# Kernel tuning notes

Measured on AMD Instinct MI355X. Metric: run time of the kernel, lower is better.

## Reference

```python
import jax, jax.numpy as jnp
import numpy as np
from jax import lax

# VGG16 conv configuration: (in_ch, out_ch) for 13 3x3 convs, blocks [2,2,3,3,3]
CONV_CFG = [(3,64),(64,64),(64,128),(128,128),(128,256),(256,256),(256,256),(256,512),(512,512),(512,512),(512,512),(512,512),(512,512)]
FC_CFG = [(512*7*7,4096),(4096,4096),(4096,1000)]
BLOCKS = [2,2,3,3,3]

def setup_inputs() -> dict:
    key = jax.random.key(0)
    ks = jax.random.split(key, 40)
    d = {"x": jax.random.normal(ks[0], (16,3,224,224), jnp.float32)}
    for i, (cin, cout) in enumerate(CONV_CFG):
        std = (2.0 / (cin * 9)) ** 0.5  # He init keeps 13-deep ReLU chain stable
        d[f"w{i+1}"] = jax.random.normal(ks[1+i], (cout, cin, 3, 3), jnp.float32) * std
        d[f"b{i+1}"] = jnp.zeros((cout,), jnp.float32)
    for j, (fin, fout) in enumerate(FC_CFG):
        std = (2.0 / fin) ** 0.5
        d[f"fw{j+1}"] = jax.random.normal(ks[20+j], (fin, fout), jnp.float32) * std
        d[f"fb{j+1}"] = jnp.zeros((fout,), jnp.float32)
    d["patch_location_tensor"] = jax.random.randint(ks[30], (16, 2), 0, 200)
    d["p_height"] = 16
    d["p_width"] = 16
    return d

def _conv_relu(x, w, b):
    # 3x3 conv, stride 1, SAME padding (pad=1), NCHW, followed by ReLU
    y = lax.conv_general_dilated(x, w, (1, 1), 'SAME', dimension_numbers=('NCHW', 'OIHW', 'NCHW'))
    return jax.nn.relu(y + b[None, :, None, None])

def _maxpool2(x):
    return lax.reduce_window(x, -jnp.inf, lax.max, (1, 1, 2, 2), (1, 1, 2, 2), 'VALID')

def reference(x, w1, b1, w2, b2, w3, b3, w4, b4, w5, b5, w6, b6, w7, b7, w8, b8, w9, b9, w10, b10, w11, b11, w12, b12, w13, b13, fw1, fb1, fw2, fb2, fw3, fb3, patch_location_tensor, p_height, p_width):
    # The incremental modules patch-update cached full-model activations; the net
    # result equals a dense VGG16 forward on x. patch_location_tensor / p_height /
    # p_width only control which region is recomputed, not the output values.
    ws = [w1, w2, w3, w4, w5, w6, w7, w8, w9, w10, w11, w12, w13]
    bs = [b1, b2, b3, b4, b5, b6, b7, b8, b9, b10, b11, b12, b13]
    h = x
    k = 0
    for n in BLOCKS:
        for _ in range(n):
            h = _conv_relu(h, ws[k], bs[k])
            k += 1
        h = _maxpool2(h)
    h = h.reshape(h.shape[0], -1)  # [B, 25088]
    h = jax.nn.relu(h @ fw1 + fb1)
    h = jax.nn.relu(h @ fw2 + fb2)
    return h @ fw3 + fb3  # [B, 1000]
```

## Files before the change

kernel.cpp:

```cpp
#include <hip/hip_runtime.h>
#include <hip/hip_bf16.h>

typedef __hip_bfloat16 bf16;
typedef __attribute__((ext_vector_type(4))) short s16x4;
typedef __attribute__((ext_vector_type(8))) short short8;
typedef __attribute__((ext_vector_type(8))) __bf16 bf16x8;
typedef __attribute__((ext_vector_type(4))) float f32x4;

__device__ __forceinline__ float s2f(short s) {
  return __builtin_bit_cast(float, (unsigned)((unsigned short)s) << 16);
}
__device__ __forceinline__ short f2s(float f) {
  return __builtin_bit_cast(short, __float2bfloat16(f));
}

__device__ __forceinline__ void gl16(const bf16* g, bf16* l) {
  __builtin_amdgcn_global_load_lds(
      (const __attribute__((address_space(1))) void*)g,
      (__attribute__((address_space(3))) void*)l, 16, 0, 0);
}

__global__ void zerofill(float* p, int n) {
  int i = blockIdx.x * 256 + threadIdx.x;
  if (i < n) p[i] = 0.f;
}

__global__ __launch_bounds__(256) void conv1_first(
    const float* __restrict__ x, const float* __restrict__ w,
    const float* __restrict__ b, bf16* __restrict__ out) {
  __shared__ float it[3][18][18];
  __shared__ float wl2[27 * 64];
  __shared__ float bl[64];
  const int tid = threadIdx.x;
  const int n = blockIdx.z;
  const int h0 = blockIdx.y * 16, w0 = blockIdx.x * 16;
  for (int i = tid; i < 1728; i += 256) {
    int jj = i >> 6, co = i & 63;
    wl2[i] = w[co * 27 + jj];
  }
  if (tid < 64) bl[tid] = b[tid];
  for (int i = tid; i < 972; i += 256) {
    int ci = i / 324; int r = i - ci * 324; int ty = r / 18, tx = r - ty * 18;
    int hh = h0 - 1 + ty, ww = w0 - 1 + tx;
    float v = 0.f;
    if (hh >= 0 && hh < 224 && ww >= 0 && ww < 224)
      v = x[((long)n * 3 + ci) * 50176 + hh * 224 + ww];
    it[ci][ty][tx] = v;
  }
  __syncthreads();
  const int ty = tid >> 4, tx = tid & 15;
  long ob = (((long)n * 224 + h0 + ty) * 224 + (w0 + tx)) * 64;
  for (int cog = 0; cog < 4; ++cog) {
    f32x4 a4[4];
    #pragma unroll
    for (int q = 0; q < 4; ++q) a4[q] = *(const f32x4*)&bl[cog * 16 + q * 4];
    #pragma unroll
    for (int jj = 0; jj < 27; ++jj) {
      const int ci = jj / 9, r = jj - ci * 9, kh = r / 3, kw = r - kh * 3;
      float v = it[ci][ty + kh][tx + kw];
      const f32x4* wp4 = (const f32x4*)&wl2[jj * 64 + cog * 16];
      #pragma unroll
      for (int q = 0; q < 4; ++q) a4[q] += v * wp4[q];
    }
    short8 s0, s1;
    #pragma unroll
    for (int u = 0; u < 4; ++u) {
      s0[u] = f2s(fmaxf(a4[0][u], 0.f));
      s0[4 + u] = f2s(fmaxf(a4[1][u], 0.f));
      s1[u] = f2s(fmaxf(a4[2][u], 0.f));
      s1[4 + u] = f2s(fmaxf(a4[3][u], 0.f));
    }
    *(short8*)(out + ob + cog * 16) = s0;
    *(short8*)(out + ob + cog * 16 + 8) = s1;
  }
}

struct RepackMeta {
  const float* src[12];
  long dstOff[12];
  int cinM1[12];
  int cshift[12];
  int cout[12];
};

__global__ __launch_bounds__(256) void repack_all(RepackMeta m, bf16* __restrict__ blob) {
  const int li = blockIdx.y;
  const int co = blockIdx.x;
  if (co >= m.cout[li]) return;
  const int cs = m.cshift[li];
  const int cinM1 = m.cinM1[li];
  const int K = 9 << cs;
  const float* src = m.src[li] + (long)co * (cinM1 + 1) * 9;
  bf16* dst = blob + m.dstOff[li] + (long)co * K;
  for (int k = threadIdx.x; k < K; k += 256) {
    int pos = k >> cs;
    int ci = k & cinM1;
    dst[k] = __float2bfloat16(src[ci * 9 + pos]);
  }
}

__global__ __launch_bounds__(256) void conv_halo64(
    const bf16* __restrict__ in, const bf16* __restrict__ wp,
    const float* __restrict__ bias, bf16* __restrict__ out,
    const bf16* __restrict__ zp) {
  __shared__ bf16 tA[10 * 34 * 64];
  __shared__ bf16 tB[9 * 64 * 64];
  const int tid = threadIdx.x;
  const int lane = tid & 63, wv = tid >> 6;
  const int n = blockIdx.z;
  const int h0 = blockIdx.y * 8, w0 = blockIdx.x * 32;

  #pragma unroll
  for (int i = 0; i < 11; ++i) {
    int cid = i * 256 + tid;
    if (cid < 2720) {
      int row = cid / 272;
      int rem = cid - row * 272;
      int w = rem >> 3, j = rem & 7;
      int hg = h0 - 1 + row, wg = w0 - 1 + w;
      bool ok = (hg >= 0) & (hg < 224) & (wg >= 0) & (wg < 224);
      const bf16* src = ok ? (in + (((long)n * 224 + hg) * 224 + wg) * 64 + ((j ^ (w & 7)) << 3))
                           : zp;
      gl16(src, tA + (long)cid * 8);
    }
  }
  {
    const int colB = tid >> 3;
    const int colx = ((tid & 7) ^ (colB & 7)) * 8;
    const bf16* s0 = wp + (long)colB * 576 + colx;
    const bf16* s1 = wp + (long)(colB + 32) * 576 + colx;
    #pragma unroll
    for (int p = 0; p < 9; ++p) {
      gl16(s0 + p * 64, tB + p * 4096 + tid * 8);
      gl16(s1 + p * 64, tB + p * 4096 + 2048 + tid * 8);
    }
  }
  __syncthreads();

  f32x4 acc[4][4];
  #pragma unroll
  for (int m = 0; m < 4; ++m)
    #pragma unroll
    for (int n2 = 0; n2 < 4; ++n2) acc[m][n2] = (f32x4){0.f, 0.f, 0.f, 0.f};

  for (int pos = 0; pos < 9; ++pos) {
    const int dh = pos / 3, dw = pos - (pos / 3) * 3;
    #pragma unroll
    for (int ks = 0; ks < 2; ++ks) {
      const int kb = ks * 64 + (lane >> 4) * 16;
      bf16x8 af[4], bfv[4];
      #pragma unroll
      for (int m = 0; m < 4; ++m) {
        int p = wv * 64 + m * 16 + (lane & 15);
        int hl = (p >> 5) + dh, wl = (p & 31) + dw;
        af[m] = *(const bf16x8*)((const char*)tA + hl * 4352 + wl * 128 + (kb ^ ((wl & 7) << 4)));
      }
      #pragma unroll
      for (int n2 = 0; n2 < 4; ++n2) {
        int c = n2 * 16 + (lane & 15);
        bfv[n2] = *(const bf16x8*)((const char*)tB + pos * 8192 + c * 128 + (kb ^ ((c & 7) << 4)));
      }
      #pragma unroll
      for (int m = 0; m < 4; ++m)
        #pragma unroll
        for (int n2 = 0; n2 < 4; ++n2)
          acc[m][n2] = __builtin_amdgcn_mfma_f32_16x16x32_bf16(af[m], bfv[n2], acc[m][n2], 0, 0, 0);
    }
  }

  const int ho = blockIdx.y * 4 + wv;
  #pragma unroll
  for (int m = 0; m < 2; ++m) {
    #pragma unroll
    for (int n2 = 0; n2 < 4; ++n2) {
      int co = n2 * 16 + (lane & 15);
      float bb = bias[co];
      #pragma unroll
      for (int qh = 0; qh < 2; ++qh) {
        int qq = 2 * qh;
        float v0 = fmaxf(acc[m][n2][qq] + bb, 0.f);
        float v1 = fmaxf(acc[m][n2][qq + 1] + bb, 0.f);
        float v2 = fmaxf(acc[m + 2][n2][qq] + bb, 0.f);
        float v3 = fmaxf(acc[m + 2][n2][qq + 1] + bb, 0.f);
        float mx = fmaxf(fmaxf(v0, v1), fmaxf(v2, v3));
        int wl = (m * 16 + ((lane >> 4) << 2) + qq) & 31;
        int wo = (w0 >> 1) + (wl >> 1);
        out[(((long)n * 112 + ho) * 112 + wo) * 64 + co] = __float2bfloat16(mx);
      }
    }
  }
}

__global__ __launch_bounds__(512) void conv_halo128p(
    const bf16* __restrict__ in, const bf16* __restrict__ wp,
    const float* __restrict__ bias, bf16* __restrict__ out,
    const bf16* __restrict__ zp) {
  __shared__ bf16 tA[18 * 18 * 128];
  __shared__ bf16 tB[2][128 * 128];
  const int tid = threadIdx.x;
  const int lane = tid & 63, wv = tid >> 6;
  const int wr = wv >> 1, wc = wv & 1;
  const int n = blockIdx.z;
  const int h0 = blockIdx.y * 16, w0 = blockIdx.x * 16;

  #pragma unroll
  for (int i = 0; i < 11; ++i) {
    int cid = i * 512 + tid;
    if (cid < 5184) {
      int row = cid / 288;
      int rem = cid - row * 288;
      int w = rem >> 4, j = rem & 15;
      int hg = h0 - 1 + row, wg = w0 - 1 + w;
      bool ok = (hg >= 0) & (hg < 112) & (wg >= 0) & (wg < 112);
      const bf16* src = ok ? (in + (((long)n * 112 + hg) * 112 + wg) * 128 + ((j ^ (w & 7)) << 3))
                           : zp;
      gl16(src, tA + (long)cid * 8);
    }
  }
  #pragma unroll
  for (int i = 0; i < 4; ++i) {
    int cid = i * 512 + tid;
    int co = cid >> 4, j = cid & 15;
    const bf16* src = wp + (long)co * 1152 + ((j ^ (co & 7)) << 3);
    gl16(src, tB[0] + (long)cid * 8);
  }
  __syncthreads();

  f32x4 acc[4][4];
  #pragma unroll
  for (int m = 0; m < 4; ++m)
    #pragma unroll
    for (int n2 = 0; n2 < 4; ++n2) acc[m][n2] = (f32x4){0.f, 0.f, 0.f, 0.f};

  for (int pos = 0; pos < 9; ++pos) {
    if (pos < 8) {
      bf16* dst = tB[(pos + 1) & 1];
      #pragma unroll
      for (int i = 0; i < 4; ++i) {
        int cid = i * 512 + tid;
        int co = cid >> 4, j = cid & 15;
        const bf16* src = wp + (long)co * 1152 + (pos + 1) * 128 + ((j ^ (co & 7)) << 3);
        gl16(src, dst + (long)cid * 8);
      }
    }
    const bf16* bB = tB[pos & 1];
    const int dh = pos / 3, dw = pos - (pos / 3) * 3;
    #pragma unroll
    for (int kq = 0; kq < 4; ++kq) {
      const int kb = kq * 64 + (lane >> 4) * 16;
      bf16x8 af[4], bfv[4];
      #pragma unroll
      for (int m = 0; m < 4; ++m) {
        int hl = wr * 4 + m + dh;
        int wl = (lane & 15) + dw;
        af[m] = *(const bf16x8*)((const char*)tA + hl * 4608 + wl * 256 + (kb ^ ((wl & 7) << 4)));
      }
      #pragma unroll
      for (int n2 = 0; n2 < 4; ++n2) {
        int c = wc * 64 + n2 * 16 + (lane & 15);
        bfv[n2] = *(const bf16x8*)((const char*)bB + c * 256 + (kb ^ ((c & 7) << 4)));
      }
      #pragma unroll
      for (int m = 0; m < 4; ++m)
        #pragma unroll
        for (int n2 = 0; n2 < 4; ++n2)
          acc[m][n2] = __builtin_amdgcn_mfma_f32_16x16x32_bf16(af[m], bfv[n2], acc[m][n2], 0, 0, 0);
    }
    __syncthreads();
  }

  const int hoB = blockIdx.y * 8, woB = blockIdx.x * 8;
  #pragma unroll
  for (int mh = 0; mh < 2; ++mh) {
    const int m = 2 * mh;
    const int ho = hoB + wr * 2 + mh;
    #pragma unroll
    for (int n2 = 0; n2 < 4; ++n2) {
      int co = wc * 64 + n2 * 16 + (lane & 15);
      float bb = bias[co];
      #pragma unroll
      for (int qh = 0; qh < 2; ++qh) {
        int qq = 2 * qh;
        float v0 = fmaxf(acc[m][n2][qq] + bb, 0.f);
        float v1 = fmaxf(acc[m][n2][qq + 1] + bb, 0.f);
        float v2 = fmaxf(acc[m + 1][n2][qq] + bb, 0.f);
        float v3 = fmaxf(acc[m + 1][n2][qq + 1] + bb, 0.f);
        float mx = fmaxf(fmaxf(v0, v1), fmaxf(v2, v3));
        int wo = woB + (lane >> 4) * 2 + qh;
        out[(((long)n * 56 + ho) * 56 + wo) * 128 + co] = __float2bfloat16(mx);
      }
    }
  }
}

template <int BM, int BN, int WM, int WN, int SPLITK>
__global__ __launch_bounds__(WM* WN * 64) void conv_gemm(
    const bf16* __restrict__ in, const bf16* __restrict__ wp,
    const float* __restrict__ bias, bf16* __restrict__ out,
    float* __restrict__ pout, const bf16* __restrict__ zp,
    int Cin, int cshift, int Cout, int H, int W, int NHW) {
  constexpr int NT = WM * WN * 64;
  constexpr int IA = BM * 8 / NT;
  constexpr int IB = BN * 8 / NT;
  __shared__ bf16 lA[BM * 64];
  __shared__ bf16 lB[BN * 64];
  const int tid = threadIdx.x;
  const int lane = tid & 63, wv = tid >> 6;
  const int wr = wv / WN, wc = wv % WN;

  const int gx = gridDim.x;
  const int nwg = gx * gridDim.y;
  const int fid = blockIdx.y * gx + blockIdx.x;
  const int q = nwg >> 3, r = nwg & 7;
  const int xcd = fid & 7, idx = fid >> 3;
  const int swz = (xcd < r ? xcd * (q + 1) : r * (q + 1) + (xcd - r) * q) + idx;
  const int p0 = (swz % gx) * BM;
  const int co0 = (swz / gx) * BN;

  const int K = 9 << cshift;
  const int HW = H * W;
  const int colx = ((tid & 7) ^ ((tid >> 3) & 7)) * 8;

  int baseA[IA]; short hA[IA], wA[IA];
  #pragma unroll
  for (int i = 0; i < IA; ++i) {
    int rr = i * (NT / 8) + (tid >> 3);
    int p = p0 + rr;
    if (p < NHW) {
      int n = p / HW; int rem = p - n * HW; int h = rem / W; int w_ = rem - h * W;
      hA[i] = (short)h; wA[i] = (short)w_;
      baseA[i] = ((n * H + h) * W + w_) * Cin;
    } else { hA[i] = -9999; wA[i] = -9999; baseA[i] = 0; }
  }

  f32x4 acc[4][4];
  #pragma unroll
  for (int m = 0; m < 4; ++m)
    #pragma unroll
    for (int n2 = 0; n2 < 4; ++n2) acc[m][n2] = (f32x4){0.f, 0.f, 0.f, 0.f};

  const int Kper = K / SPLITK;
  const int kBeg = (SPLITK > 1) ? (int)blockIdx.z * Kper : 0;
  const int kEnd = kBeg + Kper;

  const bf16* srcB[IB];
  #pragma unroll
  for (int i = 0; i < IB; ++i) {
    int col = i * (NT / 8) + (tid >> 3);
    srcB[i] = wp + (long)(co0 + col) * K + kBeg + colx;
  }

  int kk = kBeg;
  while (kk < kEnd) {
    const int pos = kk >> cshift;
    const int dh = pos / 3 - 1, dw = pos - (pos / 3) * 3 - 1;
    int posEnd = (pos + 1) << cshift;
    if (posEnd > kEnd) posEnd = kEnd;
    const bf16* srcA[IA];
    {
      const int doff = (dh * W + dw) * Cin + (kk & (Cin - 1)) + colx;
      #pragma unroll
      for (int i = 0; i < IA; ++i) {
        int hh = hA[i] + dh, ww = wA[i] + dw;
        bool ok = (hh >= 0) & (hh < H) & (ww >= 0) & (ww < W);
        srcA[i] = ok ? (in + baseA[i] + doff) : (zp + colx);
      }
    }
    for (; kk < posEnd; kk += 64) {
      __syncthreads();
      #pragma unroll
      for (int i = 0; i < IA; ++i) {
        gl16(srcA[i], lA + i * (NT * 8) + wv * 512);
        srcA[i] += 64;
      }
      #pragma unroll
      for (int i = 0; i < IB; ++i) {
        gl16(srcB[i], lB + i * (NT * 8) + wv * 512);
        srcB[i] += 64;
      }
      __syncthreads();
      #pragma unroll
      for (int ks = 0; ks < 2; ++ks) {
        const int kb = ks * 64 + (lane >> 4) * 16;
        bf16x8 af[4], bfv[4];
        #pragma unroll
        for (int m = 0; m < 4; ++m) {
          int rr = wr * 64 + m * 16 + (lane & 15);
          af[m] = *(const bf16x8*)((const char*)lA + rr * 128 + (kb ^ ((rr & 7) << 4)));
        }
        #pragma unroll
        for (int n2 = 0; n2 < 4; ++n2) {
          int c = wc * 64 + n2 * 16 + (lane & 15);
          bfv[n2] = *(const bf16x8*)((const char*)lB + c * 128 + (kb ^ ((c & 7) << 4)));
        }
        #pragma unroll
        for (int m = 0; m < 4; ++m)
          #pragma unroll
          for (int n2 = 0; n2 < 4; ++n2)
            acc[m][n2] = __builtin_amdgcn_mfma_f32_16x16x32_bf16(af[m], bfv[n2], acc[m][n2], 0, 0, 0);
      }
    }
  }

  if constexpr (SPLITK == 1) {
    #pragma unroll
    for (int m = 0; m < 4; ++m) {
      int pb = p0 + wr * 64 + m * 16 + (lane >> 4) * 4;
      #pragma unroll
      for (int n2 = 0; n2 < 4; ++n2) {
        int co = co0 + wc * 64 + n2 * 16 + (lane & 15);
        float bb = bias[co];
        #pragma unroll
        for (int qq = 0; qq < 4; ++qq) {
          int pp = pb + qq;
          if (pp < NHW)
            out[(long)pp * Cout + co] = __float2bfloat16(fmaxf(acc[m][n2][qq] + bb, 0.f));
        }
      }
    }
  } else {
    float* pb_ = pout + (long)blockIdx.z * NHW * Cout;
    #pragma unroll
    for (int m = 0; m < 4; ++m) {
      int pb = p0 + wr * 64 + m * 16 + (lane >> 4) * 4;
      #pragma unroll
      for (int n2 = 0; n2 < 4; ++n2) {
        int co = co0 + wc * 64 + n2 * 16 + (lane & 15);
        #pragma unroll
        for (int qq = 0; qq < 4; ++qq) {
          int pp = pb + qq;
          if (pp < NHW) pb_[(long)pp * Cout + co] = acc[m][n2][qq];
        }
      }
    }
  }
}

template <int NPARTS, bool POOL>
__global__ __launch_bounds__(256) void reduce_split(
    const float* __restrict__ part, const float* __restrict__ bias,
    bf16* __restrict__ out, int NHW, int H, int W, int C) {
  const long total = (long)NHW * C;
  if constexpr (!POOL) {
    long e4 = ((long)blockIdx.x * 256 + threadIdx.x) * 4;
    if (e4 >= total) return;
    f32x4 s = *(const f32x4*)(part + e4);
    #pragma unroll
    for (int p2 = 1; p2 < NPARTS; ++p2) {
      f32x4 b = *(const f32x4*)(part + (long)p2 * total + e4);
      s += b;
    }
    f32x4 bv = *(const f32x4*)(bias + (int)(e4 & (C - 1)));
    s16x4 r;
    #pragma unroll
    for (int u = 0; u < 4; ++u) r[u] = f2s(fmaxf(s[u] + bv[u], 0.f));
    *(s16x4*)(out + e4) = r;
  } else {
    const int H2 = H >> 1, W2 = W >> 1;
    long id4 = ((long)blockIdx.x * 256 + threadIdx.x) * 4;
    long ptotal = ((long)NHW / 4) * C;
    if (id4 >= ptotal) return;
    int c4 = (int)(id4 & (C - 1));
    long rest = id4 / C;
    int wo = (int)(rest % W2);
    long t2 = rest / W2;
    int ho = (int)(t2 % H2);
    int n = (int)(t2 / H2);
    f32x4 bv = *(const f32x4*)(bias + c4);
    f32x4 mx;
    #pragma unroll
    for (int dy = 0; dy < 2; ++dy)
      #pragma unroll
      for (int dx = 0; dx < 2; ++dx) {
        long p = ((long)n * H + 2 * ho + dy) * W + 2 * wo + dx;
        long e = p * C + c4;
        f32x4 s = *(const f32x4*)(part + e);
        #pragma unroll
        for (int p2 = 1; p2 < NPARTS; ++p2) {
          f32x4 b = *(const f32x4*)(part + (long)p2 * total + e);
          s += b;
        }
        s += bv;
        if (dy == 0 && dx == 0) mx = s;
        else {
          #pragma unroll
          for (int u = 0; u < 4; ++u) mx[u] = fmaxf(mx[u], s[u]);
        }
      }
    s16x4 r;
    #pragma unroll
    for (int u = 0; u < 4; ++u) r[u] = f2s(fmaxf(mx[u], 0.f));
    *(s16x4*)(out + ((long)(n * H2 + ho) * W2 + wo) * C + c4) = r;
  }
}

__global__ void maxpool_nhwc(const bf16* __restrict__ in, bf16* __restrict__ out,
                             int H, int W, int C, int cshift3, int WC8) {
  const int id = blockIdx.x * 256 + threadIdx.x;
  if (id >= WC8) return;
  const int H2 = H >> 1, W2 = W >> 1;
  const int ho = blockIdx.y, n = blockIdx.z;
  const int wo = id >> cshift3, c8 = id & ((1 << cshift3) - 1);
  const bf16* p = in + (((long)(n * H + 2 * ho) * W) + 2 * wo) * C + c8 * 8;
  short8 a = *(const short8*)p;
  short8 bq = *(const short8*)(p + C);
  short8 c = *(const short8*)(p + (long)W * C);
  short8 d = *(const short8*)(p + (long)W * C + C);
  short8 r;
  #pragma unroll
  for (int u = 0; u < 8; ++u) {
    float m = fmaxf(fmaxf(s2f(a[u]), s2f(bq[u])), fmaxf(s2f(c[u]), s2f(d[u])));
    r[u] = f2s(m);
  }
  *(short8*)(out + ((long)(n * H2 + ho) * W2 + wo) * C + c8 * 8) = r;
}

__global__ __launch_bounds__(256) void fc1_partial(
    const bf16* __restrict__ in, const float* __restrict__ w,
    float* __restrict__ part) {
  const int j0 = blockIdx.x * 1024 + threadIdx.x * 4;
  const int k0 = blockIdx.y * 128;
  __shared__ float ilds[128][16];
  #pragma unroll
  for (int i = 0; i < 8; ++i) {
    int e = i * 256 + threadIdx.x;
    int kk = e >> 4, n = e & 15;
    int k = k0 + kk;
    int cch = k / 49, s = k - cch * 49;
    ilds[kk][n] = s2f(__builtin_bit_cast(short, in[((long)n * 49 + s) * 512 + cch]));
  }
  __syncthreads();
  f32x4 acc[16];
  #pragma unroll
  for (int n = 0; n < 16; ++n) acc[n] = (f32x4){0.f, 0.f, 0.f, 0.f};
  #pragma unroll 4
  for (int kk = 0; kk < 128; ++kk) {
    f32x4 w4 = *(const f32x4*)(w + (long)(k0 + kk) * 4096 + j0);
    #pragma unroll
    for (int n = 0; n < 16; ++n) {
      float v = ilds[kk][n];
      acc[n] += v * w4;
    }
  }
  float* pp = part + (long)blockIdx.y * 16 * 4096;
  #pragma unroll
  for (int n = 0; n < 16; ++n) *(f32x4*)(pp + n * 4096 + j0) = acc[n];
}

template <int KPER>
__global__ __launch_bounds__(256) void fc23_partial(
    const float* __restrict__ in, const float* __restrict__ w,
    float* __restrict__ part, int fin, int fout) {
  const int j0 = blockIdx.x * 1024 + threadIdx.x * 4;
  const int k0 = blockIdx.y * KPER;
  __shared__ float ilds[KPER][16];
  #pragma unroll
  for (int i = 0; i < KPER / 16; ++i) {
    int e = i * 256 + threadIdx.x;
    int kk = e >> 4, n = e & 15;
    ilds[kk][n] = fmaxf(in[(long)n * fin + k0 + kk], 0.f);
  }
  __syncthreads();
  if (j0 >= fout) return;
  f32x4 acc[16];
  #pragma unroll
  for (int n = 0; n < 16; ++n) acc[n] = (f32x4){0.f, 0.f, 0.f, 0.f};
  #pragma unroll 4
  for (int kk = 0; kk < KPER; ++kk) {
    f32x4 w4 = *(const f32x4*)(w + (long)(k0 + kk) * fout + j0);
    #pragma unroll
    for (int n = 0; n < 16; ++n) {
      float v = ilds[kk][n];
      acc[n] += v * w4;
    }
  }
  float* pp = part + (long)blockIdx.y * 16 * fout;
  #pragma unroll
  for (int n = 0; n < 16; ++n) *(f32x4*)(pp + n * fout + j0) = acc[n];
}

__global__ void reduce_fc(const float* __restrict__ part, const float* __restrict__ bias,
                          float* __restrict__ out, int nparts, int fout, int total) {
  int i = blockIdx.x * 256 + threadIdx.x;
  if (i >= total) return;
  int n = i / fout, j = i - n * fout;
  float s = bias[j];
  for (int p = 0; p < nparts; ++p) s += part[((long)p * 16 + n) * fout + j];
  out[i] = s;
}

extern "C" void kernel_launch(void* const* d_in, const int* in_sizes, int n_in,
                              void* d_out, int out_size, void* d_ws, size_t ws_size,
                              hipStream_t stream) {
  const float* x = (const float*)d_in[0];
  const float* cw[13]; const float* cb[13];
  for (int i = 0; i < 13; ++i) { cw[i] = (const float*)d_in[1 + 2 * i]; cb[i] = (const float*)d_in[2 + 2 * i]; }
  const float* fw1 = (const float*)d_in[27]; const float* fb1 = (const float*)d_in[28];
  const float* fw2 = (const float*)d_in[29]; const float* fb2 = (const float*)d_in[30];
  const float* fw3 = (const float*)d_in[31]; const float* fb3 = (const float*)d_in[32];
  float* outp = (float*)d_out;

  const size_t REGION = 102760448;
  char* wsb = (char*)d_ws;
  bf16* A = (bf16*)wsb;
  bf16* B = (bf16*)(wsb + REGION);
  char* ST = wsb + 2 * REGION;
  bf16* zp = (bf16*)ST;
  bf16* WBLOB = (bf16*)(ST + 4096);
  char* ST2 = ST + 4096 + 31 * 1024 * 1024;
  float* F1 = (float*)ST2;
  float* F2 = F1 + 16 * 4096;
  float* PS = F2 + 16 * 4096;

  struct LayerCfg { int cin, cs, cout, H, W; };
  const LayerCfg L[12] = {
      {64, 6, 64, 224, 224},  {64, 6, 128, 112, 112}, {128, 7, 128, 112, 112},
      {128, 7, 256, 56, 56},  {256, 8, 256, 56, 56},  {256, 8, 256, 56, 56},
      {256, 8, 512, 28, 28},  {512, 9, 512, 28, 28},  {512, 9, 512, 28, 28},
      {512, 9, 512, 14, 14},  {512, 9, 512, 14, 14},  {512, 9, 512, 14, 14}};
  const bool poolAfter[12] = {true, false, true, false, false, true, false, false, true, false, false, true};

  RepackMeta rm;
  long off = 0;
  long offs[12];
  for (int li = 0; li < 12; ++li) {
    rm.src[li] = cw[li + 1];
    rm.cinM1[li] = L[li].cin - 1;
    rm.cshift[li] = L[li].cs;
    rm.cout[li] = L[li].cout;
    rm.dstOff[li] = off;
    offs[li] = off;
    off += (long)L[li].cout * (9 << L[li].cs);
  }
  zerofill<<<4, 256, 0, stream>>>((float*)zp, 1024);
  repack_all<<<dim3(512, 12), 256, 0, stream>>>(rm, WBLOB);

  conv1_first<<<dim3(14, 14, 16), 256, 0, stream>>>(x, cw[0], cb[0], A);

  bf16* cur = A;
  bf16* oth = B;
  for (int li = 0; li < 12; ++li) {
    const LayerCfg& c = L[li];
    bf16* wb = WBLOB + offs[li];
    const int NHW = 16 * c.H * c.W;
    const bool fusedPool = poolAfter[li] && (li == 0 || li == 2 || li >= 6);
    if (li == 0) {
      conv_halo64<<<dim3(7, 28, 16), 256, 0, stream>>>(cur, wb, cb[li + 1], oth, zp);
    } else if (li == 1) {
      conv_gemm<256, 128, 4, 2, 1><<<dim3(NHW / 256, 1), 512, 0, stream>>>(
          cur, wb, cb[li + 1], oth, nullptr, zp, c.cin, c.cs, c.cout, c.H, c.W, NHW);
    } else if (li == 2) {
      conv_halo128p<<<dim3(7, 7, 16), 512, 0, stream>>>(cur, wb, cb[li + 1], oth, zp);
    } else if (li <= 5) {
      conv_gemm<128, 256, 2, 4, 1><<<dim3(NHW / 128, 1), 512, 0, stream>>>(
          cur, wb, cb[li + 1], oth, nullptr, zp, c.cin, c.cs, c.cout, c.H, c.W, NHW);
    } else if (li <= 8) {
      conv_gemm<128, 256, 2, 4, 2><<<dim3((NHW + 127) / 128, c.cout / 256, 2), 512, 0, stream>>>(
          cur, wb, cb[li + 1], nullptr, PS, zp, c.cin, c.cs, c.cout, c.H, c.W, NHW);
      if (fusedPool) {
        long pt = ((long)NHW / 4) * c.cout;
        reduce_split<2, true><<<(int)((pt / 4 + 255) / 256), 256, 0, stream>>>(
            PS, cb[li + 1], oth, NHW, c.H, c.W, c.cout);
      } else {
        long tot = (long)NHW * c.cout;
        reduce_split<2, false><<<(int)((tot / 4 + 255) / 256), 256, 0, stream>>>(
            PS, cb[li + 1], oth, NHW, c.H, c.W, c.cout);
      }
    } else {
      conv_gemm<128, 128, 2, 2, 4><<<dim3((NHW + 127) / 128, c.cout / 128, 4), 256, 0, stream>>>(
          cur, wb, cb[li + 1], nullptr, PS, zp, c.cin, c.cs, c.cout, c.H, c.W, NHW);
      if (fusedPool) {
        long pt = ((long)NHW / 4) * c.cout;
        reduce_split<4, true><<<(int)((pt / 4 + 255) / 256), 256, 0, stream>>>(
            PS, cb[li + 1], oth, NHW, c.H, c.W, c.cout);
      } else {
        long tot = (long)NHW * c.cout;
        reduce_split<4, false><<<(int)((tot / 4 + 255) / 256), 256, 0, stream>>>(
            PS, cb[li + 1], oth, NHW, c.H, c.W, c.cout);
      }
    }
    bf16* t = cur; cur = oth; oth = t;
    if (poolAfter[li] && !fusedPool) {
      int cs3 = (c.cout == 64) ? 3 : (c.cout == 128) ? 4 : (c.cout == 256) ? 5 : 6;
      int W2 = c.W / 2, H2 = c.H / 2;
      int WC8 = W2 << cs3;
      maxpool_nhwc<<<dim3((WC8 + 255) / 256, H2, 16), 256, 0, stream>>>(cur, oth, c.H, c.W, c.cout, cs3, WC8);
      t = cur; cur = oth; oth = t;
    }
  }
  float* P1 = (float*)oth;
  float* P2 = (float*)((char*)oth + 52u * 1024 * 1024);
  float* P3 = (float*)((char*)oth + 89u * 1024 * 1024);

  fc1_partial<<<dim3(4, 196), 256, 0, stream>>>(cur, fw1, P1);
  reduce_fc<<<(16 * 4096 + 255) / 256, 256, 0, stream>>>(P1, fb1, F1, 196, 4096, 16 * 4096);
  fc23_partial<32><<<dim3(4, 128), 256, 0, stream>>>(F1, fw2, P2, 4096, 4096);
  reduce_fc<<<(16 * 4096 + 255) / 256, 256, 0, stream>>>(P2, fb2, F2, 128, 4096, 16 * 4096);
  fc23_partial<32><<<dim3(1, 128), 256, 0, stream>>>(F2, fw3, P3, 4096, 1000);
  reduce_fc<<<(16 * 1000 + 255) / 256, 256, 0, stream>>>(P3, fb3, outp, 128, 1000, 16 * 1000);
}
```

Baseline: 1.018 ms.

## Add halo-tiled implicit-GEMM kernel for the 64-to-128 channel conv layer

Replaces the generic implicit-GEMM conv path for the 112x112, 64->128 channel layer with a dedicated kernel. Each block loads an 18x18x64 input halo tile into LDS once and reuses it across all nine filter taps, while double-buffering the per-tap weight slices. The goal is to cut the repeated global/LDS loads of overlapping input windows that the im2col-style GEMM performs. In exchange it uses larger LDS per block and a fixed tile shape hardcoded to this layer's dimensions.

```diff
diff --git a/kernel.cpp b/kernel.cpp
--- a/kernel.cpp
+++ b/kernel.cpp
@@ -186,6 +186,99 @@
         int wl = (m * 16 + ((lane >> 4) << 2) + qq) & 31;
         int wo = (w0 >> 1) + (wl >> 1);
         out[(((long)n * 112 + ho) * 112 + wo) * 64 + co] = __float2bfloat16(mx);
+      }
+    }
+  }
+}
+
+__global__ __launch_bounds__(512) void conv_halo1(
+    const bf16* __restrict__ in, const bf16* __restrict__ wp,
+    const float* __restrict__ bias, bf16* __restrict__ out,
+    const bf16* __restrict__ zp) {
+  __shared__ bf16 tA[18 * 18 * 64];
+  __shared__ bf16 tB[2][128 * 64];
+  const int tid = threadIdx.x;
+  const int lane = tid & 63, wv = tid >> 6;
+  const int wr = wv >> 1, wc = wv & 1;
+  const int n = blockIdx.z;
+  const int h0 = blockIdx.y * 16, w0 = blockIdx.x * 16;
+
+  #pragma unroll
+  for (int i = 0; i < 6; ++i) {
+    int cid = i * 512 + tid;
+    if (cid < 2592) {
+      int row = cid / 144;
+      int rem = cid - row * 144;
+      int w = rem >> 3, j = rem & 7;
+      int hg = h0 - 1 + row, wg = w0 - 1 + w;
+      bool ok = (hg >= 0) & (hg < 112) & (wg >= 0) & (wg < 112);
+      const bf16* src = ok ? (in + (((long)n * 112 + hg) * 112 + wg) * 64 + ((j ^ (w & 7)) << 3))
+                           : zp;
+      gl16(src, tA + (long)cid * 8);
+    }
+  }
+  #pragma unroll
+  for (int i = 0; i < 2; ++i) {
+    int cid = i * 512 + tid;
+    int co = cid >> 3, j = cid & 7;
+    gl16(wp + (long)co * 576 + ((j ^ (co & 7)) << 3), tB[0] + (long)cid * 8);
+  }
+  __syncthreads();
+
+  f32x4 acc[4][4];
+  #pragma unroll
+  for (int m = 0; m < 4; ++m)
+    #pragma unroll
+    for (int n2 = 0; n2 < 4; ++n2) acc[m][n2] = (f32x4){0.f, 0.f, 0.f, 0.f};
+
+  for (int pos = 0; pos < 9; ++pos) {
+    if (pos < 8) {
+      bf16* dst = tB[(pos + 1) & 1];
+      #pragma unroll
+      for (int i = 0; i < 2; ++i) {
+        int cid = i * 512 + tid;
+        int co = cid >> 3, j = cid & 7;
+        gl16(wp + (long)co * 576 + (pos + 1) * 64 + ((j ^ (co & 7)) << 3), dst + (long)cid * 8);
+      }
+    }
+    const bf16* bB = tB[pos & 1];
+    const int dh = pos / 3, dw = pos - (pos / 3) * 3;
+    #pragma unroll
+    for (int ks = 0; ks < 2; ++ks) {
+      const int kb = ks * 64 + (lane >> 4) * 16;
+      bf16x8 af[4], bfv[4];
+      #pragma unroll
+      for (int m = 0; m < 4; ++m) {
+        int hl = wr * 4 + m + dh;
+        int wl = (lane & 15) + dw;
+        af[m] = *(const bf16x8*)((const char*)tA + hl * 2304 + wl * 128 + (kb ^ ((wl & 7) << 4)));
+      }
+      #pragma unroll
+      for (int n2 = 0; n2 < 4; ++n2) {
+        int c = wc * 64 + n2 * 16 + (lane & 15);
+        bfv[n2] = *(const bf16x8*)((const char*)bB + c * 128 + (kb ^ ((c & 7) << 4)));
+      }
+      #pragma unroll
+      for (int m = 0; m < 4; ++m)
+        #pragma unroll
+        for (int n2 = 0; n2 < 4; ++n2)
+          acc[m][n2] = __builtin_amdgcn_mfma_f32_16x16x32_bf16(af[m], bfv[n2], acc[m][n2], 0, 0, 0);
+    }
+    __syncthreads();
+  }
+
+  #pragma unroll
+  for (int m = 0; m < 4; ++m) {
+    const int h = h0 + wr * 4 + m;
+    #pragma unroll
+    for (int n2 = 0; n2 < 4; ++n2) {
+      int co = wc * 64 + n2 * 16 + (lane & 15);
+      float bb = bias[co];
+      #pragma unroll
+      for (int qq = 0; qq < 4; ++qq) {
+        int w = w0 + (lane >> 4) * 4 + qq;
+        out[(((long)n * 112 + h) * 112 + w) * 128 + co] =
+            __float2bfloat16(fmaxf(acc[m][n2][qq] + bb, 0.f));
       }
     }
   }
@@ -647,8 +740,7 @@
     if (li == 0) {
       conv_halo64<<<dim3(7, 28, 16), 256, 0, stream>>>(cur, wb, cb[li + 1], oth, zp);
     } else if (li == 1) {
-      conv_gemm<256, 128, 4, 2, 1><<<dim3(NHW / 256, 1), 512, 0, stream>>>(
-          cur, wb, cb[li + 1], oth, nullptr, zp, c.cin, c.cs, c.cout, c.H, c.W, NHW);
+      conv_halo1<<<dim3(7, 7, 16), 512, 0, stream>>>(cur, wb, cb[li + 1], oth, zp);
     } else if (li == 2) {
       conv_halo128p<<<dim3(7, 7, 16), 512, 0, stream>>>(cur, wb, cb[li + 1], oth, zp);
     } else if (li <= 5) {
```

Result: no change. 1.016 ms (median of 2 runs) (-0.2%).
